# Optimization experiments

Hardware: AMD Instinct MI355X
Metric: run time of the kernel (lower is better)

## Reference

```python
import jax, jax.numpy as jnp
import numpy as np


def _cos(a, b, eps):
    # cosine similarity along last axis, clamping each norm to >= eps (torch semantics)
    na = jnp.maximum(jnp.linalg.norm(a, axis=-1), eps)
    nb = jnp.maximum(jnp.linalg.norm(b, axis=-1), eps)
    return jnp.sum(a * b, axis=-1) / (na * nb)


def setup_inputs() -> dict:
    key = jax.random.key(0)
    k1, k2, k3 = jax.random.split(key, 3)
    S, B, D = 64, 256, 1024
    logits = jax.random.normal(k1, (S, B, D), dtype=jnp.float32)
    tgt_out = jax.random.normal(k2, (S, B, D), dtype=jnp.float32)
    tgt_padding_mask = jax.random.randint(k3, (B, S), 0, 2).astype(bool)
    return {"logits": logits, "tgt_out": tgt_out, "tgt_padding_mask": tgt_padding_mask}


def reference(logits, tgt_out, tgt_padding_mask):
    S, B, D = logits.shape
    f = logits.dtype
    valid = ~tgt_padding_mask                      # (B, S) True = real sentence
    valid_sb = valid.T                             # (S, B)
    n_valid = valid.sum().astype(f)

    # masked MSE over all unpadded elements (mean over n_valid * D elements)
    m = valid_sb[:, :, None]
    loss_mse = jnp.sum(jnp.square(logits - tgt_out) * m) / (n_valid * D)

    # CosineEmbeddingLoss with target = 1: mean over valid rows of (1 - cos)
    c = _cos(logits, tgt_out, 1e-8)                # (S, B)
    loss_cos = jnp.sum((1.0 - c) * valid_sb) / n_valid

    # consecutive-sentence cosine deltas, batch-major flattening (as original loops)
    lb = jnp.swapaxes(logits, 0, 1)                # (B, S, D)
    tb = jnp.swapaxes(tgt_out, 0, 1)
    pair_valid = valid[:, :-1] & valid[:, 1:]      # (B, S-1)
    d_l = _cos(lb[:, :-1], lb[:, 1:], 1e-6)        # (B, S-1)
    d_t = _cos(tb[:, :-1], tb[:, 1:], 1e-6)
    cnt = pair_valid.sum()
    loss_delta = jnp.sum(jnp.square(d_l - d_t) * pair_valid) / jnp.maximum(cnt, 1).astype(f)

    # delta-of-delta: finite differences between CONSECUTIVE entries of the
    # compacted (valid-only, batch-major) delta list. Compact via rank scatter.
    L = B * (S - 1)
    pvf = pair_valid.reshape(-1)
    rank = jnp.cumsum(pvf) - 1
    idx = jnp.where(pvf, rank, L)                  # invalid -> out-of-bounds, dropped

    def dd(d_flat):
        dense = jnp.zeros(L, d_flat.dtype).at[idx].set(d_flat, mode="drop")
        prev = dense[:-1]
        den = jnp.where(prev != 0, prev, jnp.asarray(1e-6, d_flat.dtype))
        return (dense[1:] - prev) / den            # (L-1,)

    dd_l = dd(d_l.reshape(-1))
    dd_t = dd(d_t.reshape(-1))
    dd_valid = jnp.arange(L - 1) < (cnt - 1)
    n_dd = jnp.maximum(cnt - 1, 1).astype(f)
    loss_dd = jnp.sum(jnp.square(dd_l - dd_t) * dd_valid) / n_dd / 100.0

    return loss_mse + loss_cos + loss_delta + loss_dd
```

## Files before the change

kernel.cpp:

```cpp
#include <hip/hip_runtime.h>

#define S_DIM 64
#define B_DIM 256
#define D_DIM 1024
#define BS (B_DIM * S_DIM)
#define LP (B_DIM * (S_DIM - 1))
#define NBP 128
#define PSTR 8

__device__ __forceinline__ float dot4(float4 a, float4 b) {
  return a.x * b.x + a.y * b.y + a.z * b.z + a.w * b.w;
}

template <int CTRL>
__device__ __forceinline__ float dpp_add(float v) {
  int r = __builtin_amdgcn_update_dpp(__float_as_int(v), __float_as_int(v),
                                      CTRL, 0xF, 0xF, false);
  return v + __int_as_float(r);
}

__device__ __forceinline__ float red16(float v) {
  v = dpp_add<0x128>(v);
  v = dpp_add<0x124>(v);
  v = dpp_add<0x122>(v);
  v = dpp_add<0x121>(v);
  return v;
}

__device__ __forceinline__ float red64_uni(float v) {
  v = red16(v);
  float r = __int_as_float(__builtin_amdgcn_readlane(__float_as_int(v), 0));
  r += __int_as_float(__builtin_amdgcn_readlane(__float_as_int(v), 16));
  r += __int_as_float(__builtin_amdgcn_readlane(__float_as_int(v), 32));
  r += __int_as_float(__builtin_amdgcn_readlane(__float_as_int(v), 48));
  return r;
}

__global__ __launch_bounds__(256) void row_stats_kernel(
    const float* __restrict__ logits, const float* __restrict__ tgt,
    const unsigned char* __restrict__ mask, float* __restrict__ ws) {
  const int tid = threadIdx.x;
  const int lane = tid & 63;
  int bid = blockIdx.x;
  bid = (bid & 7) * 512 + (bid >> 3);
  const int gw = (bid << 2) | (tid >> 6);
  const int h  = gw & 1;
  const int s0 = ((gw >> 1) & 31) << 1;
  const int b  = gw >> 6;

  float* nl2p = ws;
  float* nt2p = ws + 8 * BS;
  float* ltp  = ws + 16 * BS;
  float* ajlp = ws + 24 * BS;
  float* ajtp = ws + 32 * BS;

  uchar4 det = reinterpret_cast<const uchar4*>(mask)[lane];
  const bool isbyte = __ballot((det.y | det.z | det.w) != 0) != 0ull;
  auto mvalid = [&](int s) -> bool {
    const int idx = b * S_DIM + s;
    return mask[isbyte ? idx : (idx << 2)] == 0;
  };
  const bool v0 = mvalid(s0);
  const bool v1 = mvalid(s0 + 1);
  const bool vp = (s0 > 0) && mvalid(s0 - 1);
  const bool needP  = v0 && vp;
  const bool needP1 = v0 && v1;

  const int fo = h * 128 + lane;

  float4 R[4], N[4], P[4];

  auto ldrow = [&](int s, float4* dst) {
    const float4* Lp = reinterpret_cast<const float4*>(
        logits + ((size_t)s * B_DIM + b) * D_DIM);
    const float4* Tp = reinterpret_cast<const float4*>(
        tgt + ((size_t)s * B_DIM + b) * D_DIM);
    dst[0] = Lp[fo];
    dst[1] = Lp[fo + 64];
    dst[2] = Tp[fo];
    dst[3] = Tp[fo + 64];
  };

  if (v0) ldrow(s0, R);
  if (v1) ldrow(s0 + 1, N);
  if (needP) ldrow(s0 - 1, P);

  float a0 = 0.f, a1 = 0.f, a2 = 0.f, a3 = 0.f, a4 = 0.f;
  float b0 = 0.f, b1 = 0.f, b2 = 0.f, b3 = 0.f, b4 = 0.f;
  if (v0) {
    a0 = dot4(R[0], R[0]) + dot4(R[1], R[1]);
    a1 = dot4(R[2], R[2]) + dot4(R[3], R[3]);
    a2 = dot4(R[0], R[2]) + dot4(R[1], R[3]);
  }
  if (needP) {
    a3 = dot4(R[0], P[0]) + dot4(R[1], P[1]);
    a4 = dot4(R[2], P[2]) + dot4(R[3], P[3]);
  }
  if (v1) {
    b0 = dot4(N[0], N[0]) + dot4(N[1], N[1]);
    b1 = dot4(N[2], N[2]) + dot4(N[3], N[3]);
    b2 = dot4(N[0], N[2]) + dot4(N[1], N[3]);
  }
  if (needP1) {
    b3 = dot4(N[0], R[0]) + dot4(N[1], R[1]);
    b4 = dot4(N[2], R[2]) + dot4(N[3], R[3]);
  }

  if (v0) { a0 = red16(a0); a1 = red16(a1); a2 = red16(a2); }
  if (needP) { a3 = red16(a3); a4 = red16(a4); }
  if (v1) { b0 = red16(b0); b1 = red16(b1); b2 = red16(b2); }
  if (needP1) { b3 = red16(b3); b4 = red16(b4); }

  if ((lane & 15) == 0) {
    const int q = lane >> 4;
    const int i = b * S_DIM + s0;
    const int o = PSTR * i + h * 4 + q;
    if (v0) { nl2p[o] = a0; nt2p[o] = a1; ltp[o] = a2; }
    if (needP) { ajlp[o - PSTR] = a3; ajtp[o - PSTR] = a4; }
    if (v1) {
      nl2p[o + PSTR] = b0; nt2p[o + PSTR] = b1; ltp[o + PSTR] = b2;
    }
    if (needP1) { ajlp[o] = b3; ajtp[o] = b4; }
  }
}

__device__ __forceinline__ float ld8(const float* p, int i) {
  const float4* q4 = reinterpret_cast<const float4*>(p) + 2 * i;
  float4 x = q4[0], y = q4[1];
  return ((x.x + x.y) + (x.z + x.w)) + ((y.x + y.y) + (y.z + y.w));
}

__global__ __launch_bounds__(128) void pair_kernel(
    const unsigned char* __restrict__ mask, float* __restrict__ ws) {
  const float* nl2p = ws;
  const float* nt2p = ws + 8 * BS;
  const float* ltp  = ws + 16 * BS;
  const float* ajlp = ws + 24 * BS;
  const float* ajtp = ws + 32 * BS;
  float* partial = ws + 40 * BS;

  __shared__ unsigned long long vb[16];
  __shared__ float psum[6][2];
  __shared__ int s_flag;

  const int tid = threadIdx.x;
  const int w = tid >> 6, lane = tid & 63;

  if (tid == 0) s_flag = 0;
  __syncthreads();
  int any = 0;
  for (int i = tid; i < 1024; i += 128)
    if ((i & 3) == 1 && mask[i]) any = 1;
  if (any) s_flag = 1;
  __syncthreads();
  const bool isbyte = (s_flag != 0);

  int B0 = (blockIdx.x * 128) / 63;
  if (B0 > B_DIM - 16) B0 = B_DIM - 16;

#pragma unroll
  for (int k = 0; k < 8; ++k) {
    const int q = k * 2 + w;
    const int g2 = (B0 + q) * 64 + lane;
    bool val = mask[isbyte ? g2 : (g2 << 2)] == 0;
    unsigned long long bal = __ballot(val);
    if (lane == 0) vb[q] = bal;
  }
  __syncthreads();

  const int g = blockIdx.x * 128 + tid;

  float nv = 0.f, mse = 0.f, coss = 0.f, dsum = 0.f, ddsum = 0.f, cntf = 0.f;

  if (mask[isbyte ? g : (g << 2)] == 0) {
    float A = ld8(nl2p, g), Q = ld8(nt2p, g), Cc = ld8(ltp, g);
    nv = 1.f;
    mse = A + Q - 2.f * Cc;
    coss = 1.f - Cc / (fmaxf(sqrtf(A), 1e-8f) * fmaxf(sqrtf(Q), 1e-8f));
  }

  if (g < LP) {
    const int b = g / 63;
    const int s = g - b * 63;
    const unsigned long long pbb = vb[b - B0] & (vb[b - B0] >> 1);
    if ((pbb >> s) & 1ull) {
      const int i0 = b * S_DIM + s;
      float dl = ld8(ajlp, i0) / (fmaxf(sqrtf(ld8(nl2p, i0)), 1e-6f) *
                                  fmaxf(sqrtf(ld8(nl2p, i0 + 1)), 1e-6f));
      float dt = ld8(ajtp, i0) / (fmaxf(sqrtf(ld8(nt2p, i0)), 1e-6f) *
                                  fmaxf(sqrtf(ld8(nt2p, i0 + 1)), 1e-6f));
      float wv = dl - dt;
      dsum = wv * wv;
      cntf = 1.f;

      int bq = b, sq = -1;
      bool found = false, fellback = false;
      unsigned long long cur = pbb & (~0ull << (s + 1));
      while (true) {
        if (cur) { sq = __builtin_ctzll(cur); found = true; break; }
        ++bq;
        if (bq >= B_DIM) break;
        if (bq - B0 < 16) {
          cur = vb[bq - B0] & (vb[bq - B0] >> 1);
        } else {
          fellback = true;
          break;
        }
      }
      if (fellback) {
        while (bq < B_DIM && !found) {
          for (int s2 = 0; s2 < 63; ++s2) {
            int r0 = bq * S_DIM + s2;
            bool q1 = mask[isbyte ? r0 : (r0 << 2)] == 0;
            bool q2 = mask[isbyte ? (r0 + 1) : ((r0 + 1) << 2)] == 0;
            if (q1 && q2) { sq = s2; found = true; break; }
          }
          if (!found) ++bq;
        }
      }
      if (found) {
        const int j0 = bq * S_DIM + sq;
        float dlq = ld8(ajlp, j0) / (fmaxf(sqrtf(ld8(nl2p, j0)), 1e-6f) *
                                     fmaxf(sqrtf(ld8(nl2p, j0 + 1)), 1e-6f));
        float dtq = ld8(ajtp, j0) / (fmaxf(sqrtf(ld8(nt2p, j0)), 1e-6f) *
                                     fmaxf(sqrtf(ld8(nt2p, j0 + 1)), 1e-6f));
        float ddl = (dlq - dl) / ((dl != 0.f) ? dl : 1e-6f);
        float ddt = (dtq - dt) / ((dt != 0.f) ? dt : 1e-6f);
        float u = ddl - ddt;
        ddsum = u * u;
      }
    }
  }

  float vals[6] = {nv, mse, coss, dsum, ddsum, cntf};
#pragma unroll
  for (int k2 = 0; k2 < 6; ++k2) {
    float v = red64_uni(vals[k2]);
    if (lane == 0) psum[k2][w] = v;
  }
  __syncthreads();
  if (tid == 0) {
#pragma unroll
    for (int k2 = 0; k2 < 6; ++k2)
      partial[k2 * NBP + blockIdx.x] = psum[k2][0] + psum[k2][1];
  }
}

__global__ __launch_bounds__(128) void final_combine_kernel(
    const float* __restrict__ ws, float* __restrict__ out) {
  const float* partial = ws + 40 * BS;
  __shared__ float sm[6][2];
  const int tid = threadIdx.x, w = tid >> 6, lane = tid & 63;
#pragma unroll
  for (int k = 0; k < 6; ++k) {
    float v = red64_uni(partial[k * NBP + tid]);
    if (lane == 0) sm[k][w] = v;
  }
  __syncthreads();
  if (tid == 0) {
    float nv   = sm[0][0] + sm[0][1];
    float mse  = sm[1][0] + sm[1][1];
    float coss = sm[2][0] + sm[2][1];
    float dsum = sm[3][0] + sm[3][1];
    float ddsm = sm[4][0] + sm[4][1];
    float cnt  = sm[5][0] + sm[5][1];
    out[0] = mse / (nv * (float)D_DIM) + coss / nv +
             dsum / fmaxf(cnt, 1.f) + (ddsm / fmaxf(cnt - 1.f, 1.f)) * 0.01f;
  }
}

extern "C" void kernel_launch(void* const* d_in, const int* in_sizes, int n_in,
                              void* d_out, int out_size, void* d_ws, size_t ws_size,
                              hipStream_t stream) {
  const float* logits = (const float*)d_in[0];
  const float* tgt    = (const float*)d_in[1];
  const unsigned char* mask = (const unsigned char*)d_in[2];
  float* out = (float*)d_out;
  float* ws  = (float*)d_ws;

  row_stats_kernel<<<dim3(4096), dim3(256), 0, stream>>>(logits, tgt, mask, ws);
  pair_kernel<<<dim3(NBP), dim3(128), 0, stream>>>(mask, ws);
  final_combine_kernel<<<dim3(1), dim3(128), 0, stream>>>(ws, out);
}
```

Before: 29.38 us.

## Fuse final combine into pair kernel via last-block atomic counter

Drops the separate single-block final_combine launch. Each pair_kernel block now bumps an atomic counter after writing its partials, and the last block to finish does the final reduction and writes the output. The counter is reset by block 0 of row_stats_kernel, which is safe because the kernels run in stream order. It also loads both possible mask encodings up front, rather than waiting on the ballot-based detection, so the load latency overlaps. This costs a threadfence and an atomic per block.

Result: slower. 34.70 us (+18.1%).

```diff
diff --git a/kernel.cpp b/kernel.cpp
--- a/kernel.cpp
+++ b/kernel.cpp
@@ -36,11 +36,18 @@
   return r;
 }
 
+#define WS_PART (40 * BS)
+#define WS_CNT  (WS_PART + 6 * NBP)
+
 __global__ __launch_bounds__(256) void row_stats_kernel(
     const float* __restrict__ logits, const float* __restrict__ tgt,
     const unsigned char* __restrict__ mask, float* __restrict__ ws) {
   const int tid = threadIdx.x;
   const int lane = tid & 63;
+
+  if (blockIdx.x == 0 && tid == 0)
+    reinterpret_cast<int*>(ws + WS_CNT)[0] = 0;
+
   int bid = blockIdx.x;
   bid = (bid & 7) * 512 + (bid >> 3);
   const int gw = (bid << 2) | (tid >> 6);
@@ -54,15 +61,20 @@
   float* ajlp = ws + 24 * BS;
   float* ajtp = ws + 32 * BS;
 
+  const int ib = b * S_DIM;
+  const int sp = (s0 > 0) ? s0 - 1 : s0;
+  const unsigned char mA0 = mask[ib + s0];
+  const unsigned char mB0 = mask[(ib + s0) << 2];
+  const unsigned char mA1 = mask[ib + s0 + 1];
+  const unsigned char mB1 = mask[(ib + s0 + 1) << 2];
+  const unsigned char mAp = mask[ib + sp];
+  const unsigned char mBp = mask[(ib + sp) << 2];
   uchar4 det = reinterpret_cast<const uchar4*>(mask)[lane];
   const bool isbyte = __ballot((det.y | det.z | det.w) != 0) != 0ull;
-  auto mvalid = [&](int s) -> bool {
-    const int idx = b * S_DIM + s;
-    return mask[isbyte ? idx : (idx << 2)] == 0;
-  };
-  const bool v0 = mvalid(s0);
-  const bool v1 = mvalid(s0 + 1);
-  const bool vp = (s0 > 0) && mvalid(s0 - 1);
+
+  const bool v0 = (isbyte ? mA0 : mB0) == 0;
+  const bool v1 = (isbyte ? mA1 : mB1) == 0;
+  const bool vp = (s0 > 0) && ((isbyte ? mAp : mBp) == 0);
   const bool needP  = v0 && vp;
   const bool needP1 = v0 && v1;
 
@@ -131,13 +143,15 @@
 }
 
 __global__ __launch_bounds__(128) void pair_kernel(
-    const unsigned char* __restrict__ mask, float* __restrict__ ws) {
+    const unsigned char* __restrict__ mask, float* __restrict__ ws,
+    float* __restrict__ out) {
   const float* nl2p = ws;
   const float* nt2p = ws + 8 * BS;
   const float* ltp  = ws + 16 * BS;
   const float* ajlp = ws + 24 * BS;
   const float* ajtp = ws + 32 * BS;
-  float* partial = ws + 40 * BS;
+  float* partial = ws + WS_PART;
+  int* cnt = reinterpret_cast<int*>(ws + WS_CNT);
 
   __shared__ unsigned long long vb[16];
   __shared__ float psum[6][2];
@@ -244,28 +258,35 @@
     for (int k2 = 0; k2 < 6; ++k2)
       partial[k2 * NBP + blockIdx.x] = psum[k2][0] + psum[k2][1];
   }
-}
-
-__global__ __launch_bounds__(128) void final_combine_kernel(
-    const float* __restrict__ ws, float* __restrict__ out) {
-  const float* partial = ws + 40 * BS;
-  __shared__ float sm[6][2];
-  const int tid = threadIdx.x, w = tid >> 6, lane = tid & 63;
+
+  __threadfence();
+  __shared__ int s_last;
+  if (tid == 0) {
+    int prev = __hip_atomic_fetch_add(cnt, 1, __ATOMIC_ACQ_REL,
+                                      __HIP_MEMORY_SCOPE_AGENT);
+    s_last = (prev == NBP - 1);
+  }
+  __syncthreads();
+  if (!s_last) return;
+
+  float acc[6];
 #pragma unroll
-  for (int k = 0; k < 6; ++k) {
-    float v = red64_uni(partial[k * NBP + tid]);
-    if (lane == 0) sm[k][w] = v;
+  for (int k2 = 0; k2 < 6; ++k2) {
+    float v = __hip_atomic_load(&partial[k2 * NBP + tid], __ATOMIC_RELAXED,
+                                __HIP_MEMORY_SCOPE_AGENT);
+    v = red64_uni(v);
+    if (lane == 0) psum[k2][w] = v;
   }
   __syncthreads();
   if (tid == 0) {
-    float nv   = sm[0][0] + sm[0][1];
-    float mse  = sm[1][0] + sm[1][1];
-    float coss = sm[2][0] + sm[2][1];
-    float dsum = sm[3][0] + sm[3][1];
-    float ddsm = sm[4][0] + sm[4][1];
-    float cnt  = sm[5][0] + sm[5][1];
-    out[0] = mse / (nv * (float)D_DIM) + coss / nv +
-             dsum / fmaxf(cnt, 1.f) + (ddsm / fmaxf(cnt - 1.f, 1.f)) * 0.01f;
+    float nvT  = psum[0][0] + psum[0][1];
+    float mseT = psum[1][0] + psum[1][1];
+    float cosT = psum[2][0] + psum[2][1];
+    float dT   = psum[3][0] + psum[3][1];
+    float ddT  = psum[4][0] + psum[4][1];
+    float cT   = psum[5][0] + psum[5][1];
+    out[0] = mseT / (nvT * (float)D_DIM) + cosT / nvT +
+             dT / fmaxf(cT, 1.f) + (ddT / fmaxf(cT - 1.f, 1.f)) * 0.01f;
   }
 }
 
@@ -279,6 +300,5 @@
   float* ws  = (float*)d_ws;
 
   row_stats_kernel<<<dim3(4096), dim3(256), 0, stream>>>(logits, tgt, mask, ws);
-  pair_kernel<<<dim3(NBP), dim3(128), 0, stream>>>(mask, ws);
-  final_combine_kernel<<<dim3(1), dim3(128), 0, stream>>>(ws, out);
-}
+  pair_kernel<<<dim3(NBP), dim3(128), 0, stream>>>(mask, ws, out);
+}
```
